# Kernel tuning notes

Hardware: AMD Instinct MI355X
Metric: run time of the kernel (lower is better)

The kernel has to match this reference:

```python
import jax, jax.numpy as jnp
import numpy as np


def setup_inputs() -> dict:
    key = jax.random.key(0)
    k1, k2, k3 = jax.random.split(key, 3)
    B, C, O, NF = 4, 16, 16, 9  # num_flows fixed at 9 (3x3 stencil)
    x = jax.random.normal(k1, (B, C, 450, 480), dtype=jnp.float32)
    combinator = jax.random.normal(k2, (O, C * NF), dtype=jnp.float32) * 0.05
    bias = jax.random.normal(k3, (O,), dtype=jnp.float32) * 0.05
    return {"x": x, "combinator": combinator, "bias": bias}


def reference(x, combinator, bias):
    # Original forward: zero-pad x by 1, gather the 9 shifted copies
    # (dy,dx) in row-major order over {-1,0,1}^2, flatten (flow, channel)
    # flow-major, then matmul with combinator and add bias.
    # out[b,o,h,w] = sum_{i,c} combinator[o, i*C + c] * x[b,c,h+dy_i,w+dx_i]
    # with flow index i = (dy+1)*3 + (dx+1) = ky*3 + kx, this is exactly a
    # 3x3 cross-correlation (padding=1) with weight[o,c,ky,kx] =
    # combinator[o, (ky*3+kx)*C + c].
    O = combinator.shape[0]
    C = x.shape[1]
    w = combinator.reshape(O, 3, 3, C).transpose(0, 3, 1, 2)  # OIHW
    out = jax.lax.conv_general_dilated(
        x, w,
        window_strides=(1, 1),
        padding=((1, 1), (1, 1)),
        dimension_numbers=("NCHW", "OIHW", "NCHW"),
    )
    return out + bias[None, :, None, None]
```

## Files before the change

kernel.cpp:

```cpp
#include <hip/hip_runtime.h>


#define HH 450
#define WW 480
#define BB 4
#define CC 16
#define OO 16
#define WT    96
#define WQN   5
#define WIN   104
#define RSTG  14
#define ROUT  12
#define HG    38
#define NTILE 6
#define W2N   (WIN / 2)
#define HALFI (RSTG * W2N)
#define ITEMS (2 * HALFI)
#define NBLK  (BB * WQN * HG)

typedef __attribute__((ext_vector_type(8))) short    bf16x8;
typedef __attribute__((ext_vector_type(4))) float    f32x4;
typedef __attribute__((ext_vector_type(4))) unsigned u32x4;

static __device__ __forceinline__ unsigned cvt_pk_bf16(float a, float b) {
    unsigned r;
    asm("v_cvt_pk_bf16_f32 %0, %1, %2" : "=v"(r) : "v"(a), "v"(b));
    return r;
}

__global__ __launch_bounds__(256, 3) void flow_mfma_kernel(
    const float* __restrict__ x, const float* __restrict__ comb,
    const float* __restrict__ bias, float* __restrict__ out)
{
    __shared__ __align__(16) short xs[2][RSTG * WIN][8];

    const int tid  = threadIdx.x;
    const int lane = tid & 63;
    const int wv   = tid >> 6;

    int bid = blockIdx.x;
    int L   = (bid & 7) * 95 + (bid >> 3);
    int hg  = L % HG;
    int t2  = L / HG;
    int wq  = t2 % WQN;
    int b   = t2 / WQN;
    int h0  = hg * ROUT;
    int w0  = wq * WT;

    const int col = lane & 15;
    const int grp = lane >> 4;
    bf16x8 af[5];
    #pragma unroll
    for (int m = 0; m < 5; ++m) {
        int k0 = m * 32 + grp * 8;
        u32x4 p;
        if (k0 < 144) {
            float4 u = *(const float4*)(comb + col * 144 + k0);
            float4 v = *(const float4*)(comb + col * 144 + k0 + 4);
            p[0] = cvt_pk_bf16(u.x, u.y);
            p[1] = cvt_pk_bf16(u.z, u.w);
            p[2] = cvt_pk_bf16(v.x, v.y);
            p[3] = cvt_pk_bf16(v.z, v.w);
        } else {
            p[0] = p[1] = p[2] = p[3] = 0u;
        }
        af[m] = __builtin_bit_cast(bf16x8, p);
    }
    f32x4 bv = *(const f32x4*)(bias + grp * 4);

    auto stage = [&](int s) {
        int ch  = (s >= HALFI) ? 1 : 0;
        int rem = s - ch * HALFI;
        int r   = rem / W2N;
        int wi2 = rem - r * W2N;
        int hy  = h0 - 1 + r;
        int w   = w0 - 4 + wi2 * 2;
        u32x4 p0, p1;
        if (((unsigned)hy < (unsigned)HH) && ((unsigned)w < (unsigned)WW)) {
            const float* xp = x + (((size_t)(b * CC + ch * 8) * HH + hy) * WW + w);
            float fx[8], fy[8];
            #pragma unroll
            for (int j = 0; j < 8; ++j) {
                float2 v = *(const float2*)(xp + (size_t)j * HH * WW);
                fx[j] = v.x; fy[j] = v.y;
            }
            p0[0] = cvt_pk_bf16(fx[0], fx[1]);
            p0[1] = cvt_pk_bf16(fx[2], fx[3]);
            p0[2] = cvt_pk_bf16(fx[4], fx[5]);
            p0[3] = cvt_pk_bf16(fx[6], fx[7]);
            p1[0] = cvt_pk_bf16(fy[0], fy[1]);
            p1[1] = cvt_pk_bf16(fy[2], fy[3]);
            p1[2] = cvt_pk_bf16(fy[4], fy[5]);
            p1[3] = cvt_pk_bf16(fy[6], fy[7]);
        } else {
            p0[0] = p0[1] = p0[2] = p0[3] = 0u;
            p1[0] = p1[1] = p1[2] = p1[3] = 0u;
        }
        int r2 = r * WIN + wi2 * 2;
        *(u32x4*)(&xs[ch][r2][0])     = p0;
        *(u32x4*)(&xs[ch][r2 + 1][0]) = p1;
    };
    #pragma unroll
    for (int it = 0; it < 5; ++it)
        stage(tid + it * 256);
    if (tid < ITEMS - 5 * 256)
        stage(tid + 5 * 256);
    __syncthreads();

    const int fo = grp >> 1;
    const int ch = grp & 1;
    #pragma unroll
    for (int rr = 0; rr < 3; ++rr) {
        int r = 3 * wv + rr;
        int h = h0 + r;
        if (h >= HH) continue;

        int boff[5];
        #pragma unroll
        for (int m = 0; m < 4; ++m) {
            int i  = 2 * m + fo;
            int ky = i / 3;
            int kx = i % 3;
            boff[m] = (r + ky) * WIN + col + kx + 3;
        }
        boff[4] = (r + 2) * WIN + col + 2 + 3;

        #pragma unroll
        for (int t = 0; t < NTILE; ++t) {
            int n0 = t * 16;
            f32x4 acc = bv;
            #pragma unroll
            for (int m = 0; m < 4; ++m) {
                bf16x8 bf = *(const bf16x8*)(&xs[ch][boff[m] + n0][0]);
                acc = __builtin_amdgcn_mfma_f32_16x16x32_bf16(af[m], bf, acc, 0, 0, 0);
            }
            bf16x8 b4;
            if (grp < 2) {
                b4 = *(const bf16x8*)(&xs[ch][boff[4] + n0][0]);
            } else {
                #pragma unroll
                for (int j = 0; j < 8; ++j) b4[j] = 0;
            }
            acc = __builtin_amdgcn_mfma_f32_16x16x32_bf16(af[4], b4, acc, 0, 0, 0);

            float* op = out + (((size_t)(b * OO + grp * 4) * HH + h) * WW + w0 + n0 + col);
            #pragma unroll
            for (int j = 0; j < 4; ++j)
                op[(size_t)j * HH * WW] = acc[j];
        }
    }
}

extern "C" void kernel_launch(void* const* d_in, const int* in_sizes, int n_in,
                              void* d_out, int out_size, void* d_ws, size_t ws_size,
                              hipStream_t stream) {
    const float* x    = (const float*)d_in[0];
    const float* comb = (const float*)d_in[1];
    const float* bias = (const float*)d_in[2];
    float* out        = (float*)d_out;

    flow_mfma_kernel<<<NBLK, 256, 0, stream>>>(x, comb, bias, out);
}
```

Before: 25.04 us.

## Split input staging into two phases to overlap loads with MFMA compute

```diff
diff --git a/kernel.cpp b/kernel.cpp
--- a/kernel.cpp
+++ b/kernel.cpp
@@ -11,11 +11,15 @@
 #define WIN   104
 #define RSTG  14
 #define ROUT  12
+#define GR    6
 #define HG    38
 #define NTILE 6
-#define W2N   (WIN / 2)
-#define HALFI (RSTG * W2N)
-#define ITEMS (2 * HALFI)
+#define W2N   52
+#define HALF_A  (8 * W2N)
+#define ITEMS_A (2 * HALF_A)
+#define HALF_B  (6 * W2N)
+#define ITEMS_B (2 * HALF_B)
+#define PLANE   (RSTG * WIN)
 #define NBLK  (BB * WQN * HG)
 
 typedef __attribute__((ext_vector_type(8))) short    bf16x8;
@@ -32,7 +36,7 @@
     const float* __restrict__ x, const float* __restrict__ comb,
     const float* __restrict__ bias, float* __restrict__ out)
 {
-    __shared__ __align__(16) short xs[2][RSTG * WIN][8];
+    __shared__ __align__(16) short xs[2 * PLANE][8];
 
     const int tid  = threadIdx.x;
     const int lane = tid & 63;
@@ -68,75 +72,99 @@
     }
     f32x4 bv = *(const f32x4*)(bias + grp * 4);
 
-    auto stage = [&](int s) {
-        int ch  = (s >= HALFI) ? 1 : 0;
-        int rem = s - ch * HALFI;
+    const int fo = grp >> 1;
+    const int ch = grp & 1;
+    int cof[5];
+    #pragma unroll
+    for (int m = 0; m < 4; ++m) {
+        int i  = 2 * m + fo;
+        int ky = i / 3;
+        int kx = i - ky * 3;
+        cof[m] = ch * PLANE + ky * WIN + col + kx + 3;
+    }
+    cof[4] = ch * PLANE + 2 * WIN + col + 5;
+
+    auto stageA = [&](int s) {
+        int cs  = (s >= HALF_A) ? 1 : 0;
+        int rem = s - cs * HALF_A;
         int r   = rem / W2N;
         int wi2 = rem - r * W2N;
         int hy  = h0 - 1 + r;
         int w   = w0 - 4 + wi2 * 2;
         u32x4 p0, p1;
         if (((unsigned)hy < (unsigned)HH) && ((unsigned)w < (unsigned)WW)) {
-            const float* xp = x + (((size_t)(b * CC + ch * 8) * HH + hy) * WW + w);
+            const float* xp = x + (((size_t)(b * CC + cs * 8) * HH + hy) * WW + w);
             float fx[8], fy[8];
             #pragma unroll
             for (int j = 0; j < 8; ++j) {
                 float2 v = *(const float2*)(xp + (size_t)j * HH * WW);
                 fx[j] = v.x; fy[j] = v.y;
             }
-            p0[0] = cvt_pk_bf16(fx[0], fx[1]);
-            p0[1] = cvt_pk_bf16(fx[2], fx[3]);
-            p0[2] = cvt_pk_bf16(fx[4], fx[5]);
-            p0[3] = cvt_pk_bf16(fx[6], fx[7]);
-            p1[0] = cvt_pk_bf16(fy[0], fy[1]);
-            p1[1] = cvt_pk_bf16(fy[2], fy[3]);
-            p1[2] = cvt_pk_bf16(fy[4], fy[5]);
-            p1[3] = cvt_pk_bf16(fy[6], fy[7]);
+            p0[0] = cvt_pk_bf16(fx[0], fx[1]); p0[1] = cvt_pk_bf16(fx[2], fx[3]);
+            p0[2] = cvt_pk_bf16(fx[4], fx[5]); p0[3] = cvt_pk_bf16(fx[6], fx[7]);
+            p1[0] = cvt_pk_bf16(fy[0], fy[1]); p1[1] = cvt_pk_bf16(fy[2], fy[3]);
+            p1[2] = cvt_pk_bf16(fy[4], fy[5]); p1[3] = cvt_pk_bf16(fy[6], fy[7]);
         } else {
             p0[0] = p0[1] = p0[2] = p0[3] = 0u;
             p1[0] = p1[1] = p1[2] = p1[3] = 0u;
         }
-        int r2 = r * WIN + wi2 * 2;
-        *(u32x4*)(&xs[ch][r2][0])     = p0;
-        *(u32x4*)(&xs[ch][r2 + 1][0]) = p1;
+        int r2 = cs * PLANE + r * WIN + wi2 * 2;
+        *(u32x4*)(&xs[r2][0])     = p0;
+        *(u32x4*)(&xs[r2 + 1][0]) = p1;
     };
     #pragma unroll
-    for (int it = 0; it < 5; ++it)
-        stage(tid + it * 256);
-    if (tid < ITEMS - 5 * 256)
-        stage(tid + 5 * 256);
+    for (int it = 0; it < 3; ++it)
+        stageA(tid + it * 256);
+    if (tid < ITEMS_A - 3 * 256)
+        stageA(tid + 3 * 256);
+
+    float fa[3][8], fb[3][8];
+    int   wofs[3];
+    #pragma unroll
+    for (int it = 0; it < 3; ++it) {
+        int s   = tid + it * 256;
+        bool act = (s < ITEMS_B);
+        int cs  = (s >= HALF_B) ? 1 : 0;
+        int rem = s - cs * HALF_B;
+        int r   = rem / W2N;
+        int wi2 = rem - r * W2N;
+        int hy  = h0 + 7 + r;
+        int w   = w0 - 4 + wi2 * 2;
+        wofs[it] = act ? (cs * PLANE + (8 + r) * WIN + wi2 * 2) : -1;
+        if (act && (hy < HH) && ((unsigned)w < (unsigned)WW)) {
+            const float* xp = x + (((size_t)(b * CC + cs * 8) * HH + hy) * WW + w);
+            #pragma unroll
+            for (int j = 0; j < 8; ++j) {
+                float2 v = *(const float2*)(xp + (size_t)j * HH * WW);
+                fa[it][j] = v.x; fb[it][j] = v.y;
+            }
+        } else {
+            #pragma unroll
+            for (int j = 0; j < 8; ++j) { fa[it][j] = 0.0f; fb[it][j] = 0.0f; }
+        }
+    }
     __syncthreads();
 
-    const int fo = grp >> 1;
-    const int ch = grp & 1;
-    #pragma unroll
-    for (int rr = 0; rr < 3; ++rr) {
-        int r = 3 * wv + rr;
-        int h = h0 + r;
-        if (h >= HH) continue;
-
-        int boff[5];
+    auto compute = [&](int g) {
         #pragma unroll
-        for (int m = 0; m < 4; ++m) {
-            int i  = 2 * m + fo;
-            int ky = i / 3;
-            int kx = i % 3;
-            boff[m] = (r + ky) * WIN + col + kx + 3;
-        }
-        boff[4] = (r + 2) * WIN + col + 2 + 3;
-
-        #pragma unroll
-        for (int t = 0; t < NTILE; ++t) {
+        for (int k = 0; k < 9; ++k) {
+            int idx = wv + 4 * k;
+            int row = idx / 6;
+            int t   = idx - row * 6;
+            int rs  = g * GR + row;
+            int h   = h0 + rs;
+            if (h >= HH) continue;
             int n0 = t * 16;
+            int rbase = rs * WIN + n0;
             f32x4 acc = bv;
             #pragma unroll
             for (int m = 0; m < 4; ++m) {
-                bf16x8 bf = *(const bf16x8*)(&xs[ch][boff[m] + n0][0]);
+                bf16x8 bf = *(const bf16x8*)(&xs[rbase + cof[m]][0]);
                 acc = __builtin_amdgcn_mfma_f32_16x16x32_bf16(af[m], bf, acc, 0, 0, 0);
             }
             bf16x8 b4;
             if (grp < 2) {
-                b4 = *(const bf16x8*)(&xs[ch][boff[4] + n0][0]);
+                b4 = *(const bf16x8*)(&xs[rbase + cof[4]][0]);
             } else {
                 #pragma unroll
                 for (int j = 0; j < 8; ++j) b4[j] = 0;
@@ -148,7 +176,29 @@
             for (int j = 0; j < 4; ++j)
                 op[(size_t)j * HH * WW] = acc[j];
         }
-    }
+    };
+
+    compute(0);
+
+    #pragma unroll
+    for (int it = 0; it < 3; ++it) {
+        if (wofs[it] >= 0) {
+            u32x4 p0, p1;
+            p0[0] = cvt_pk_bf16(fa[it][0], fa[it][1]);
+            p0[1] = cvt_pk_bf16(fa[it][2], fa[it][3]);
+            p0[2] = cvt_pk_bf16(fa[it][4], fa[it][5]);
+            p0[3] = cvt_pk_bf16(fa[it][6], fa[it][7]);
+            p1[0] = cvt_pk_bf16(fb[it][0], fb[it][1]);
+            p1[1] = cvt_pk_bf16(fb[it][2], fb[it][3]);
+            p1[2] = cvt_pk_bf16(fb[it][4], fb[it][5]);
+            p1[3] = cvt_pk_bf16(fb[it][6], fb[it][7]);
+            *(u32x4*)(&xs[wofs[it]][0])     = p0;
+            *(u32x4*)(&xs[wofs[it] + 1][0]) = p1;
+        }
+    }
+    __syncthreads();
+
+    compute(1);
 }
 
 extern "C" void kernel_launch(void* const* d_in, const int* in_sizes, int n_in,
```

New measurement: 26.46 us. +5.7%, slower.
